# Kernel optimization log

Measured on AMD Instinct MI355X. Metric: run time of the kernel, lower is better.

The kernel has to match this reference:

```python
import jax, jax.numpy as jnp
import numpy as np

NUM_EMB = 8192
EMB_DIM = 32
LATENT = 1024
COMMIT = 0.25
CB_COST = 1.0


def _l2norm(x, eps=1e-12):
    # matches torch F.normalize: x / max(||x||, eps)
    n = jnp.sqrt(jnp.sum(x * x, axis=-1, keepdims=True))
    return x / jnp.maximum(n, eps)


def setup_inputs() -> dict:
    key = jax.random.key(0)
    k = jax.random.split(key, 6)
    B = 32768
    s_in = 1.0 / np.sqrt(LATENT)
    s_out = 1.0 / np.sqrt(EMB_DIM)
    return {
        "z_e": jax.random.normal(k[0], (B, LATENT), jnp.float32),
        "in_w": jax.random.uniform(k[1], (EMB_DIM, LATENT), jnp.float32, -s_in, s_in),
        "in_b": jax.random.uniform(k[2], (EMB_DIM,), jnp.float32, -s_in, s_in),
        "out_w": jax.random.uniform(k[3], (LATENT, EMB_DIM), jnp.float32, -s_out, s_out),
        "out_b": jax.random.uniform(k[4], (LATENT,), jnp.float32, -s_out, s_out),
        "codebook": jax.random.normal(k[5], (NUM_EMB, EMB_DIM), jnp.float32),
    }


def reference(z_e, in_w, in_b, out_w, out_b, codebook):
    # in_proj: [B, LATENT] -> [B, EMB_DIM]
    ze = z_e @ in_w.T + in_b
    zn = _l2norm(ze)                      # [B, E]
    wn = _l2norm(codebook)                # [Z, E]
    # squared euclidean distance between normalized vectors
    dist = (jnp.sum(zn * zn, axis=1, keepdims=True)
            - 2.0 * (zn @ wn.T)
            + jnp.sum(wn * wn, axis=1))   # [B, Z]
    idx = jnp.argmin(dist, axis=1)        # [B]
    z_q = codebook[idx]                   # [B, E] (unnormalized codebook lookup)
    enc_loss = jnp.mean((ze - jax.lax.stop_gradient(z_q)) ** 2)
    cb_loss = jnp.mean((z_q - jax.lax.stop_gradient(ze)) ** 2)
    loss = CB_COST * cb_loss + COMMIT * enc_loss
    # straight-through estimator
    z_st = ze + jax.lax.stop_gradient(z_q - ze)
    out = z_st @ out_w.T + out_b          # [B, LATENT]
    return out, loss, enc_loss, cb_loss, idx, ze
```

## Files before the change

kernel.cpp:

```cpp
#include <hip/hip_runtime.h>
#include <hip/hip_bf16.h>

#define B_SZ    32768
#define LAT     1024
#define EMB     32
#define ZCB     8192
#define NSPL    8
#define RESC_CAP 32768
#define EPS_MARGIN 2e-4f

#define OFF_LOSS  ((size_t)B_SZ * LAT)
#define OFF_ENC   (OFF_LOSS + 1)
#define OFF_CB    (OFF_LOSS + 2)
#define OFF_IDX   (OFF_LOSS + 3)
#define OFF_ZE    (OFF_IDX + B_SZ)

#define WS_PZE    0
#define WS_PB1    0
#define WS_PB2    262144
#define WS_PL15   524288
#define WS_CAND   1048576
#define WS_OTH    1081344
#define WS_ZEA    2097152
#define WS_ZNPK   3145728
#define WS_WPK    4194304
#define WS_IDXT   4456448
#define WS_CNT    4489216
#define WS_LIST   4489217
#define WS_LPART  4521985

typedef float  f32x4  __attribute__((ext_vector_type(4)));
typedef short  short8 __attribute__((ext_vector_type(8)));

__device__ __forceinline__ unsigned short f2bf(float x) {
    unsigned u = __float_as_uint(x);
    u += 0x7FFF + ((u >> 16) & 1);
    return (unsigned short)(u >> 16);
}
__device__ __forceinline__ float bf2f(unsigned short h) {
    return __uint_as_float(((unsigned)h) << 16);
}

__global__ __launch_bounds__(256) void knorm(const float* __restrict__ cb,
                                             short* __restrict__ wpk) {
    int e = threadIdx.x;
    int r = threadIdx.y;
    int row = blockIdx.x * 8 + r;
    float v = cb[row * EMB + e];
    float s = v * v;
    #pragma unroll
    for (int m = 16; m >= 1; m >>= 1) s += __shfl_xor(s, m, 64);
    float n = fmaxf(sqrtf(s), 1e-12f);
    float w = v / n;
    unsigned short h = f2bf(w);
    unsigned short l = f2bf(w - bf2f(h));
    wpk[row * 64 + e]      = (short)h;
    wpk[row * 64 + 32 + e] = (short)l;
}

#define KZB 64
#define KZS 68
__global__ __launch_bounds__(256) void kze2(const float* __restrict__ z_e,
                                            const float* __restrict__ in_w,
                                            float* __restrict__ pze) {
    __shared__ float zs[128 * KZS];
    __shared__ float wt[KZB * 32];
    int tid = threadIdx.x;
    size_t row0 = (size_t)blockIdx.x * 128;
    int ks = blockIdx.y;
    int rs = tid >> 2;
    int eg = tid & 3;
    int E  = eg * 8;

    float acc[2][8];
    #pragma unroll
    for (int i = 0; i < 2; ++i)
        #pragma unroll
        for (int j = 0; j < 8; ++j) acc[i][j] = 0.f;

    for (int c = 0; c < 512 / KZB; ++c) {
        int kb = ks * 512 + c * KZB;
        __syncthreads();
        #pragma unroll
        for (int i = 0; i < 8; ++i) {
            int t = tid + i * 256;
            int r = t >> 4, c4 = t & 15;
            float4 v = *(const float4*)(z_e + (row0 + r) * LAT + kb + c4 * 4);
            *(float4*)&zs[r * KZS + c4 * 4] = v;
        }
        #pragma unroll
        for (int i = 0; i < 2; ++i) {
            int t = tid + i * 256;
            int e = t >> 4, k4 = t & 15;
            float4 v = *(const float4*)(in_w + (size_t)e * LAT + kb + k4 * 4);
            float vv[4] = {v.x, v.y, v.z, v.w};
            #pragma unroll
            for (int j = 0; j < 4; ++j) {
                int k = k4 * 4 + j;
                wt[k * 32 + (e ^ ((k & 7) << 2))] = vv[j];
            }
        }
        __syncthreads();
        #pragma unroll 4
        for (int kq = 0; kq < KZB / 4; ++kq) {
            int k0 = kq * 4;
            float4 za = *(const float4*)&zs[rs * KZS + k0];
            float4 zb = *(const float4*)&zs[(rs + 64) * KZS + k0];
            float zav[4] = {za.x, za.y, za.z, za.w};
            float zbv[4] = {zb.x, zb.y, zb.z, zb.w};
            #pragma unroll
            for (int i = 0; i < 4; ++i) {
                int k = k0 + i;
                int sw = (k & 7) << 2;
                float4 w0 = *(const float4*)&wt[k * 32 + (E ^ sw)];
                float4 w1 = *(const float4*)&wt[k * 32 + ((E + 4) ^ sw)];
                float wa[8] = {w0.x, w0.y, w0.z, w0.w, w1.x, w1.y, w1.z, w1.w};
                #pragma unroll
                for (int j = 0; j < 8; ++j) {
                    acc[0][j] = fmaf(zav[i], wa[j], acc[0][j]);
                    acc[1][j] = fmaf(zbv[i], wa[j], acc[1][j]);
                }
            }
        }
    }
    size_t rb = ((size_t)ks * B_SZ + row0);
    float* p0 = pze + (rb + rs) * EMB + E;
    float* p1 = pze + (rb + rs + 64) * EMB + E;
    *(float4*)p0       = make_float4(acc[0][0], acc[0][1], acc[0][2], acc[0][3]);
    *(float4*)(p0 + 4) = make_float4(acc[0][4], acc[0][5], acc[0][6], acc[0][7]);
    *(float4*)p1       = make_float4(acc[1][0], acc[1][1], acc[1][2], acc[1][3]);
    *(float4*)(p1 + 4) = make_float4(acc[1][4], acc[1][5], acc[1][6], acc[1][7]);
}

__global__ __launch_bounds__(256) void kprep(const float* __restrict__ pze,
                                             const float* __restrict__ in_b,
                                             float* __restrict__ ze_out,
                                             float* __restrict__ ze_a,
                                             short* __restrict__ znpk) {
    int tid = threadIdx.x;
    size_t row = (size_t)blockIdx.x * 64 + (tid >> 2);
    int eg = tid & 3;
    const float* p0 = pze + row * 32 + eg * 8;
    const float* p1 = p0 + (size_t)B_SZ * 32;
    float4 a0 = *(const float4*)p0, a1 = *(const float4*)(p0 + 4);
    float4 b0 = *(const float4*)p1, b1 = *(const float4*)(p1 + 4);
    float4 c0 = *(const float4*)(in_b + eg * 8), c1 = *(const float4*)(in_b + eg * 8 + 4);
    float v[8];
    v[0] = a0.x + b0.x + c0.x; v[1] = a0.y + b0.y + c0.y;
    v[2] = a0.z + b0.z + c0.z; v[3] = a0.w + b0.w + c0.w;
    v[4] = a1.x + b1.x + c1.x; v[5] = a1.y + b1.y + c1.y;
    v[6] = a1.z + b1.z + c1.z; v[7] = a1.w + b1.w + c1.w;
    float nn = 0.f;
    #pragma unroll
    for (int i = 0; i < 8; ++i) nn = fmaf(v[i], v[i], nn);
    nn += __shfl_xor(nn, 1, 64);
    nn += __shfl_xor(nn, 2, 64);
    float n = fmaxf(sqrtf(nn), 1e-12f);

    *(float4*)(ze_a + row * 32 + eg * 8)     = make_float4(v[0], v[1], v[2], v[3]);
    *(float4*)(ze_a + row * 32 + eg * 8 + 4) = make_float4(v[4], v[5], v[6], v[7]);
    #pragma unroll
    for (int i = 0; i < 8; ++i) ze_out[row * 32 + eg * 8 + i] = v[i];

    short8 hv, lv;
    #pragma unroll
    for (int i = 0; i < 8; ++i) {
        float x = v[i] / n;
        unsigned short h = f2bf(x);
        unsigned short l = f2bf(x - bf2f(h));
        hv[i] = (short)h; lv[i] = (short)l;
    }
    *(short8*)(znpk + row * 64 + eg * 8)      = hv;
    *(short8*)(znpk + row * 64 + 32 + eg * 8) = lv;
}

__global__ __launch_bounds__(256) void kdistM(const short* __restrict__ znpk,
                                              const short* __restrict__ wpk,
                                              float* __restrict__ pb1,
                                              float* __restrict__ pb2,
                                              int*   __restrict__ pl15) {
    int tid = threadIdx.x;
    int wave = tid >> 6, l = tid & 63;
    int l15 = l & 15, g = l >> 4;
    size_t rowbase = (size_t)blockIdx.x * 256 + wave * 64;
    int s = blockIdx.y;

    short8 zh[4], zl[4];
    #pragma unroll
    for (int rt = 0; rt < 4; ++rt) {
        const short8* p = (const short8*)(znpk + (rowbase + rt * 16 + l15) * 64 + g * 8);
        zh[rt] = p[0];
        zl[rt] = p[4];
    }
    f32x4 zero4 = {0.f, 0.f, 0.f, 0.f};
    float bb1[16];
    #pragma unroll
    for (int i = 0; i < 16; ++i) bb1[i] = -1e30f;

    const short* wbase = wpk + ((size_t)s * 1024 + l15) * 64 + g * 8;
    for (int t = 0; t < 64; ++t) {
        const short8* wp = (const short8*)(wbase + (size_t)t * 1024);
        short8 bh = wp[0];
        short8 bl = wp[4];
        #pragma unroll
        for (int rt = 0; rt < 4; ++rt) {
            f32x4 acc = __builtin_amdgcn_mfma_f32_16x16x32_bf16(zh[rt], bh, zero4, 0, 0, 0);
            acc = __builtin_amdgcn_mfma_f32_16x16x32_bf16(zl[rt], bh, acc, 0, 0, 0);
            acc = __builtin_amdgcn_mfma_f32_16x16x32_bf16(zh[rt], bl, acc, 0, 0, 0);
            #pragma unroll
            for (int r = 0; r < 4; ++r) {
                int slot = rt * 4 + r;
                bb1[slot] = fmaxf(bb1[slot], acc[r]);
            }
        }
    }
    #pragma unroll
    for (int slot = 0; slot < 16; ++slot) {
        float B1 = bb1[slot], B2 = -1e30f;
        int ID = l15;
        #pragma unroll
        for (int m = 1; m <= 8; m <<= 1) {
            float ob1 = __shfl_xor(B1, m, 64);
            float ob2 = __shfl_xor(B2, m, 64);
            int   oid = __shfl_xor(ID, m, 64);
            float mn = fminf(B1, ob1);
            B2 = fmaxf(fmaxf(B2, ob2), mn);
            bool take = (ob1 > B1) || (ob1 == B1 && oid < ID);
            B1 = take ? ob1 : B1;
            ID = take ? oid : ID;
        }
        if (l15 == 0) {
            size_t row = rowbase + (size_t)(slot >> 2) * 16 + g * 4 + (slot & 3);
            pb1[(size_t)s * B_SZ + row] = B1;
            pb2[(size_t)s * B_SZ + row] = B2;
            pl15[(size_t)s * B_SZ + row] = ID;
        }
    }
}

__global__ __launch_bounds__(256) void kmergeArg(const float* __restrict__ pb1,
                                                 const float* __restrict__ pb2,
                                                 const int* __restrict__ pl15,
                                                 int* __restrict__ cand,
                                                 float* __restrict__ oth) {
    int row = blockIdx.x * 256 + threadIdx.x;
    float best1 = pb1[row], best2 = pb2[row];
    int c = pl15[row], wsn = 0;
    #pragma unroll
    for (int s = 1; s < NSPL; ++s) {
        float b  = pb1[(size_t)s * B_SZ + row];
        float sb = pb2[(size_t)s * B_SZ + row];
        int   li = pl15[(size_t)s * B_SZ + row];
        float mn = fminf(best1, b);
        best2 = fmaxf(fmaxf(best2, sb), mn);
        if (b > best1) { best1 = b; c = li; wsn = s; }
    }
    cand[row] = wsn * 16 + c;
    oth[row] = best2;
}

__global__ __launch_bounds__(256) void krecover(const float* __restrict__ ze_a,
                                                const float* __restrict__ cb,
                                                const int* __restrict__ cand,
                                                const float* __restrict__ oth,
                                                int* __restrict__ idxt,
                                                int* __restrict__ cnt,
                                                int* __restrict__ list) {
    int tid = threadIdx.x;
    int l = tid & 63;
    int gl = l & 7;
    int gj = l >> 3;
    int row = (blockIdx.x * 256 + tid) >> 6;
    int c = cand[row];
    int s = c >> 4, lc = c & 15;
    float4 z = *(const float4*)(ze_a + (size_t)row * 32 + gl * 4);
    float zz = fmaf(z.x, z.x, fmaf(z.y, z.y, fmaf(z.z, z.z, z.w * z.w)));
    zz += __shfl_xor(zz, 1, 64);
    zz += __shfl_xor(zz, 2, 64);
    zz += __shfl_xor(zz, 4, 64);
    float zinv = 1.f / fmaxf(sqrtf(zz), 1e-12f);
    z.x *= zinv; z.y *= zinv; z.z *= zinv; z.w *= zinv;

    float best = -1e30f; int bi = 0;
    #pragma unroll
    for (int b = 0; b < 8; ++b) {
        int t = b * 8 + gj;
        int j = s * 1024 + t * 16 + lc;
        float4 w = *(const float4*)(cb + (size_t)j * 32 + gl * 4);
        float w2 = fmaf(w.x, w.x, fmaf(w.y, w.y, fmaf(w.z, w.z, w.w * w.w)));
        float dt = fmaf(z.x, w.x, fmaf(z.y, w.y, fmaf(z.z, w.z, z.w * w.w)));
        w2 += __shfl_xor(w2, 1, 64); dt += __shfl_xor(dt, 1, 64);
        w2 += __shfl_xor(w2, 2, 64); dt += __shfl_xor(dt, 2, 64);
        w2 += __shfl_xor(w2, 4, 64); dt += __shfl_xor(dt, 4, 64);
        float inv = 1.f / fmaxf(sqrtf(w2), 1e-12f);
        float m = dt * inv - 0.5f * (w2 * inv * inv);
        if (m > best || (m == best && j < bi)) { best = m; bi = j; }
    }
    #pragma unroll
    for (int mk = 8; mk <= 32; mk <<= 1) {
        float ob = __shfl_xor(best, mk, 64);
        int   oi = __shfl_xor(bi, mk, 64);
        bool take = (ob > best) || (ob == best && oi < bi);
        best = take ? ob : best;
        bi   = take ? oi : bi;
    }
    if (l == 0) {
        idxt[row] = bi;
        if (best - (oth[row] - 0.5f) < EPS_MARGIN) {
            int p = atomicAdd(cnt, 1);
            if (p < RESC_CAP) list[p] = row;
        }
    }
}

__global__ __launch_bounds__(256) void krescore(const float* __restrict__ ze_a,
                                                const float* __restrict__ cb,
                                                int* __restrict__ idxt,
                                                const int* __restrict__ cnt,
                                                const int* __restrict__ list) {
    __shared__ float bvs[4];
    __shared__ int   bis[4];
    int tid = threadIdx.x;
    int wave = tid >> 6, l = tid & 63;
    int gl = l & 7;
    int gj = l >> 3;
    int n = *cnt; if (n > RESC_CAP) n = RESC_CAP;
    for (int ii = blockIdx.x; ii < n; ii += gridDim.x) {
        int row = list[ii];
        float4 z = *(const float4*)(ze_a + (size_t)row * 32 + gl * 4);
        float zz = fmaf(z.x, z.x, fmaf(z.y, z.y, fmaf(z.z, z.z, z.w * z.w)));
        zz += __shfl_xor(zz, 1, 64);
        zz += __shfl_xor(zz, 2, 64);
        zz += __shfl_xor(zz, 4, 64);
        float zinv = 1.f / fmaxf(sqrtf(zz), 1e-12f);
        z.x *= zinv; z.y *= zinv; z.z *= zinv; z.w *= zinv;

        float best = -1e30f; int bi = 0;
        int jbase = wave * 2048 + gj;
        for (int b = 0; b < 32; ++b) {
            float w2v[8], dtv[8];
            #pragma unroll
            for (int cc = 0; cc < 8; ++cc) {
                int j = jbase + (b * 8 + cc) * 8;
                float4 w = *(const float4*)(cb + (size_t)j * 32 + gl * 4);
                w2v[cc] = fmaf(w.x, w.x, fmaf(w.y, w.y, fmaf(w.z, w.z, w.w * w.w)));
                dtv[cc] = fmaf(z.x, w.x, fmaf(z.y, w.y, fmaf(z.z, w.z, z.w * w.w)));
            }
            #pragma unroll
            for (int cc = 0; cc < 8; ++cc) {
                w2v[cc] += __shfl_xor(w2v[cc], 1, 64);
                dtv[cc] += __shfl_xor(dtv[cc], 1, 64);
            }
            #pragma unroll
            for (int cc = 0; cc < 8; ++cc) {
                w2v[cc] += __shfl_xor(w2v[cc], 2, 64);
                dtv[cc] += __shfl_xor(dtv[cc], 2, 64);
            }
            #pragma unroll
            for (int cc = 0; cc < 8; ++cc) {
                w2v[cc] += __shfl_xor(w2v[cc], 4, 64);
                dtv[cc] += __shfl_xor(dtv[cc], 4, 64);
            }
            #pragma unroll
            for (int cc = 0; cc < 8; ++cc) {
                int j = jbase + (b * 8 + cc) * 8;
                float inv = 1.f / fmaxf(sqrtf(w2v[cc]), 1e-12f);
                float m = dtv[cc] * inv - 0.5f * (w2v[cc] * inv * inv);
                if (m > best || (m == best && j < bi)) { best = m; bi = j; }
            }
        }
        #pragma unroll
        for (int mk = 8; mk <= 32; mk <<= 1) {
            float ob = __shfl_xor(best, mk, 64);
            int   oi = __shfl_xor(bi, mk, 64);
            bool take = (ob > best) || (ob == best && oi < bi);
            best = take ? ob : best;
            bi   = take ? oi : bi;
        }
        if (l == 0) { bvs[wave] = best; bis[wave] = bi; }
        __syncthreads();
        if (tid == 0) {
            float B = bvs[0]; int I = bis[0];
            #pragma unroll
            for (int w2i = 1; w2i < 4; ++w2i) {
                float ob = bvs[w2i]; int oi = bis[w2i];
                if (ob > B || (ob == B && oi < I)) { B = ob; I = oi; }
            }
            idxt[row] = I;
        }
        __syncthreads();
    }
}

__global__ __launch_bounds__(256) void kfinal(const int* __restrict__ idxt,
                                              const float* __restrict__ ze,
                                              const float* __restrict__ cb,
                                              float* __restrict__ out_idx,
                                              float* __restrict__ lpart) {
    int tid = threadIdx.x;
    int row = blockIdx.x * 256 + tid;
    int bidx = idxt[row];
    out_idx[row] = (float)bidx;

    const float4* zq4 = (const float4*)(cb + (size_t)bidx * EMB);
    const float4* ze4 = (const float4*)(ze + (size_t)row * EMB);
    float sq = 0.f;
    #pragma unroll
    for (int i = 0; i < 8; ++i) {
        float4 q = zq4[i], z = ze4[i];
        float dx = z.x - q.x, dy = z.y - q.y, dz = z.z - q.z, dw = z.w - q.w;
        sq += (dx * dx + dy * dy) + (dz * dz + dw * dw);
    }
    #pragma unroll
    for (int m = 1; m <= 32; m <<= 1) sq += __shfl_xor(sq, m, 64);
    __shared__ float red[4];
    if ((tid & 63) == 0) red[tid >> 6] = sq;
    __syncthreads();
    if (tid == 0) lpart[blockIdx.x] = (red[0] + red[1]) + (red[2] + red[3]);
}

__global__ void kloss(const float* __restrict__ lpart, float* __restrict__ dout) {
    float v = lpart[threadIdx.x];
    #pragma unroll
    for (int m = 1; m <= 32; m <<= 1) v += __shfl_xor(v, m, 64);
    __shared__ float tmp[2];
    if ((threadIdx.x & 63) == 0) tmp[threadIdx.x >> 6] = v;
    __syncthreads();
    if (threadIdx.x == 0) {
        float enc = (tmp[0] + tmp[1]) / (float)(B_SZ * EMB);
        dout[OFF_LOSS] = 1.0f * enc + 0.25f * enc;
        dout[OFF_ENC]  = enc;
        dout[OFF_CB]   = enc;
    }
}

__global__ __launch_bounds__(256) void kout(const float* __restrict__ ze_a,
                                            const int* __restrict__ idxt,
                                            const float* __restrict__ cb,
                                            const float* __restrict__ out_w,
                                            const float* __restrict__ out_b,
                                            float* __restrict__ out) {
    __shared__ float zsh[128 * EMB];
    __shared__ int ish[128];
    int tid = threadIdx.x;
    int col = blockIdx.x * 512 + tid * 2;
    size_t row0 = (size_t)blockIdx.y * 128;
    if (tid < 128) ish[tid] = idxt[row0 + tid];
    __syncthreads();
    #pragma unroll
    for (int i = 0; i < 4; ++i) {
        int flat = i * 256 + tid;
        int r = flat >> 3, q = flat & 7;
        float4 zv = *(const float4*)(ze_a + (row0 + r) * EMB + q * 4);
        float4 qv = *(const float4*)(cb + (size_t)ish[r] * EMB + q * 4);
        float4 o;
        o.x = zv.x + (qv.x - zv.x); o.y = zv.y + (qv.y - zv.y);
        o.z = zv.z + (qv.z - zv.z); o.w = zv.w + (qv.w - zv.w);
        *(float4*)&zsh[r * EMB + q * 4] = o;
    }
    float wa[32], wb[32];
    {
        const float4* wa4 = (const float4*)(out_w + (size_t)col * EMB);
        const float4* wb4 = (const float4*)(out_w + (size_t)(col + 1) * EMB);
        #pragma unroll
        for (int i = 0; i < 8; ++i) {
            float4 a = wa4[i]; wa[4*i]=a.x; wa[4*i+1]=a.y; wa[4*i+2]=a.z; wa[4*i+3]=a.w;
            float4 b = wb4[i]; wb[4*i]=b.x; wb[4*i+1]=b.y; wb[4*i+2]=b.z; wb[4*i+3]=b.w;
        }
    }
    float b0 = out_b[col], b1 = out_b[col + 1];
    __syncthreads();
    for (int rr = 0; rr < 128; ++rr) {
        const float4* zr4 = (const float4*)(zsh + rr * EMB);
        float a0 = b0, a1 = b1;
        #pragma unroll
        for (int q = 0; q < 8; ++q) {
            float4 z = zr4[q];
            a0 = fmaf(z.x, wa[4*q],   a0); a1 = fmaf(z.x, wb[4*q],   a1);
            a0 = fmaf(z.y, wa[4*q+1], a0); a1 = fmaf(z.y, wb[4*q+1], a1);
            a0 = fmaf(z.z, wa[4*q+2], a0); a1 = fmaf(z.z, wb[4*q+2], a1);
            a0 = fmaf(z.w, wa[4*q+3], a0); a1 = fmaf(z.w, wb[4*q+3], a1);
        }
        float2 o; o.x = a0; o.y = a1;
        *(float2*)(out + (row0 + rr) * LAT + col) = o;
    }
}

extern "C" void kernel_launch(void* const* d_in, const int* in_sizes, int n_in,
                              void* d_out, int out_size, void* d_ws, size_t ws_size,
                              hipStream_t stream) {
    const float* z_e   = (const float*)d_in[0];
    const float* in_w  = (const float*)d_in[1];
    const float* in_b  = (const float*)d_in[2];
    const float* out_w = (const float*)d_in[3];
    const float* out_b = (const float*)d_in[4];
    const float* cb    = (const float*)d_in[5];

    float* out = (float*)d_out;
    float* ws  = (float*)d_ws;
    float* pze   = ws + WS_PZE;
    float* pb1   = ws + WS_PB1;
    float* pb2   = ws + WS_PB2;
    int*   pl15  = (int*)(ws + WS_PL15);
    int*   cand  = (int*)(ws + WS_CAND);
    float* oth   = ws + WS_OTH;
    float* ze_a  = ws + WS_ZEA;
    short* znpk  = (short*)(ws + WS_ZNPK);
    short* wpk   = (short*)(ws + WS_WPK);
    int*   idxt  = (int*)(ws + WS_IDXT);
    int*   cnt   = (int*)(ws + WS_CNT);
    int*   list  = (int*)(ws + WS_LIST);
    float* lpart = ws + WS_LPART;

    hipMemsetAsync((void*)cnt, 0, sizeof(int), stream);
    knorm    <<<dim3(ZCB / 8), dim3(32, 8), 0, stream>>>(cb, wpk);
    kze2     <<<dim3(B_SZ / 128, 2), 256, 0, stream>>>(z_e, in_w, pze);
    kprep    <<<dim3(B_SZ / 64), 256, 0, stream>>>(pze, in_b, out + OFF_ZE, ze_a, znpk);
    kdistM   <<<dim3(B_SZ / 256, NSPL), 256, 0, stream>>>(znpk, wpk, pb1, pb2, pl15);
    kmergeArg<<<dim3(B_SZ / 256), 256, 0, stream>>>(pb1, pb2, pl15, cand, oth);
    krecover <<<dim3(B_SZ / 4), 256, 0, stream>>>(ze_a, cb, cand, oth, idxt, cnt, list);
    krescore <<<dim3(512), 256, 0, stream>>>(ze_a, cb, idxt, cnt, list);
    kfinal   <<<dim3(B_SZ / 256), 256, 0, stream>>>(idxt, ze_a, cb, out + OFF_IDX, lpart);
    kloss    <<<1, 128, 0, stream>>>(lpart, out);
    kout     <<<dim3(2, B_SZ / 128), 256, 0, stream>>>(ze_a, idxt, cb, out_w, out_b, out);
}
```

Baseline: 271.6 us.

## Prefetch codebook tiles in distance loop, shrink projection tiles, fold counter reset

After: 274.3 us. No clear change (+1.0%).

```diff
diff --git a/kernel.cpp b/kernel.cpp
--- a/kernel.cpp
+++ b/kernel.cpp
@@ -6,6 +6,7 @@
 #define EMB     32
 #define ZCB     8192
 #define NSPL    8
+#define CPS     (ZCB / NSPL)
 #define RESC_CAP 32768
 #define EPS_MARGIN 2e-4f
 
@@ -19,8 +20,8 @@
 #define WS_PB1    0
 #define WS_PB2    262144
 #define WS_PL15   524288
-#define WS_CAND   1048576
-#define WS_OTH    1081344
+#define WS_CAND   786432
+#define WS_OTH    819200
 #define WS_ZEA    2097152
 #define WS_ZNPK   3145728
 #define WS_WPK    4194304
@@ -63,26 +64,24 @@
 __global__ __launch_bounds__(256) void kze2(const float* __restrict__ z_e,
                                             const float* __restrict__ in_w,
                                             float* __restrict__ pze) {
-    __shared__ float zs[128 * KZS];
+    __shared__ float zs[64 * KZS];
     __shared__ float wt[KZB * 32];
     int tid = threadIdx.x;
-    size_t row0 = (size_t)blockIdx.x * 128;
+    size_t row0 = (size_t)blockIdx.x * 64;
     int ks = blockIdx.y;
     int rs = tid >> 2;
     int eg = tid & 3;
     int E  = eg * 8;
 
-    float acc[2][8];
-    #pragma unroll
-    for (int i = 0; i < 2; ++i)
-        #pragma unroll
-        for (int j = 0; j < 8; ++j) acc[i][j] = 0.f;
+    float acc[8];
+    #pragma unroll
+    for (int j = 0; j < 8; ++j) acc[j] = 0.f;
 
     for (int c = 0; c < 512 / KZB; ++c) {
         int kb = ks * 512 + c * KZB;
         __syncthreads();
         #pragma unroll
-        for (int i = 0; i < 8; ++i) {
+        for (int i = 0; i < 4; ++i) {
             int t = tid + i * 256;
             int r = t >> 4, c4 = t & 15;
             float4 v = *(const float4*)(z_e + (row0 + r) * LAT + kb + c4 * 4);
@@ -105,9 +104,7 @@
         for (int kq = 0; kq < KZB / 4; ++kq) {
             int k0 = kq * 4;
             float4 za = *(const float4*)&zs[rs * KZS + k0];
-            float4 zb = *(const float4*)&zs[(rs + 64) * KZS + k0];
             float zav[4] = {za.x, za.y, za.z, za.w};
-            float zbv[4] = {zb.x, zb.y, zb.z, zb.w};
             #pragma unroll
             for (int i = 0; i < 4; ++i) {
                 int k = k0 + i;
@@ -116,20 +113,15 @@
                 float4 w1 = *(const float4*)&wt[k * 32 + ((E + 4) ^ sw)];
                 float wa[8] = {w0.x, w0.y, w0.z, w0.w, w1.x, w1.y, w1.z, w1.w};
                 #pragma unroll
-                for (int j = 0; j < 8; ++j) {
-                    acc[0][j] = fmaf(zav[i], wa[j], acc[0][j]);
-                    acc[1][j] = fmaf(zbv[i], wa[j], acc[1][j]);
-                }
-            }
-        }
-    }
-    size_t rb = ((size_t)ks * B_SZ + row0);
+                for (int j = 0; j < 8; ++j)
+                    acc[j] = fmaf(zav[i], wa[j], acc[j]);
+            }
+        }
+    }
+    size_t rb = (size_t)ks * B_SZ + row0;
     float* p0 = pze + (rb + rs) * EMB + E;
-    float* p1 = pze + (rb + rs + 64) * EMB + E;
-    *(float4*)p0       = make_float4(acc[0][0], acc[0][1], acc[0][2], acc[0][3]);
-    *(float4*)(p0 + 4) = make_float4(acc[0][4], acc[0][5], acc[0][6], acc[0][7]);
-    *(float4*)p1       = make_float4(acc[1][0], acc[1][1], acc[1][2], acc[1][3]);
-    *(float4*)(p1 + 4) = make_float4(acc[1][4], acc[1][5], acc[1][6], acc[1][7]);
+    *(float4*)p0       = make_float4(acc[0], acc[1], acc[2], acc[3]);
+    *(float4*)(p0 + 4) = make_float4(acc[4], acc[5], acc[6], acc[7]);
 }
 
 __global__ __launch_bounds__(256) void kprep(const float* __restrict__ pze,
@@ -197,22 +189,29 @@
     #pragma unroll
     for (int i = 0; i < 16; ++i) bb1[i] = -1e30f;
 
-    const short* wbase = wpk + ((size_t)s * 1024 + l15) * 64 + g * 8;
-    for (int t = 0; t < 64; ++t) {
-        const short8* wp = (const short8*)(wbase + (size_t)t * 1024);
-        short8 bh = wp[0];
-        short8 bl = wp[4];
+    const short* wbase = wpk + ((size_t)s * CPS + l15) * 64 + g * 8;
+    const short8* wp0 = (const short8*)wbase;
+    short8 bh = wp0[0];
+    short8 bl = wp0[4];
+    for (int t = 0; t < CPS / 16; ++t) {
+        short8 nbh = bh, nbl = bl;
+        if (t + 1 < CPS / 16) {
+            const short8* wn = (const short8*)(wbase + (size_t)(t + 1) * 1024);
+            nbh = wn[0];
+            nbl = wn[4];
+        }
         #pragma unroll
         for (int rt = 0; rt < 4; ++rt) {
-            f32x4 acc = __builtin_amdgcn_mfma_f32_16x16x32_bf16(zh[rt], bh, zero4, 0, 0, 0);
-            acc = __builtin_amdgcn_mfma_f32_16x16x32_bf16(zl[rt], bh, acc, 0, 0, 0);
-            acc = __builtin_amdgcn_mfma_f32_16x16x32_bf16(zh[rt], bl, acc, 0, 0, 0);
+            f32x4 c1 = __builtin_amdgcn_mfma_f32_16x16x32_bf16(zh[rt], bh, zero4, 0, 0, 0);
+            f32x4 c2 = __builtin_amdgcn_mfma_f32_16x16x32_bf16(zh[rt], bl, zero4, 0, 0, 0);
+            c2 = __builtin_amdgcn_mfma_f32_16x16x32_bf16(zl[rt], bh, c2, 0, 0, 0);
             #pragma unroll
             for (int r = 0; r < 4; ++r) {
                 int slot = rt * 4 + r;
-                bb1[slot] = fmaxf(bb1[slot], acc[r]);
-            }
-        }
+                bb1[slot] = fmaxf(bb1[slot], c1[r] + c2[r]);
+            }
+        }
+        bh = nbh; bl = nbl;
     }
     #pragma unroll
     for (int slot = 0; slot < 16; ++slot) {
@@ -242,7 +241,9 @@
                                                  const float* __restrict__ pb2,
                                                  const int* __restrict__ pl15,
                                                  int* __restrict__ cand,
-                                                 float* __restrict__ oth) {
+                                                 float* __restrict__ oth,
+                                                 int* __restrict__ cnt) {
+    if (blockIdx.x == 0 && threadIdx.x == 0) *cnt = 0;
     int row = blockIdx.x * 256 + threadIdx.x;
     float best1 = pb1[row], best2 = pb2[row];
     int c = pl15[row], wsn = 0;
@@ -283,9 +284,9 @@
 
     float best = -1e30f; int bi = 0;
     #pragma unroll
-    for (int b = 0; b < 8; ++b) {
+    for (int b = 0; b < CPS / 16 / 8; ++b) {
         int t = b * 8 + gj;
-        int j = s * 1024 + t * 16 + lc;
+        int j = s * CPS + t * 16 + lc;
         float4 w = *(const float4*)(cb + (size_t)j * 32 + gl * 4);
         float w2 = fmaf(w.x, w.x, fmaf(w.y, w.y, fmaf(w.z, w.z, w.w * w.w)));
         float dt = fmaf(z.x, w.x, fmaf(z.y, w.y, fmaf(z.z, w.z, z.w * w.w)));
@@ -512,12 +513,11 @@
     int*   list  = (int*)(ws + WS_LIST);
     float* lpart = ws + WS_LPART;
 
-    hipMemsetAsync((void*)cnt, 0, sizeof(int), stream);
     knorm    <<<dim3(ZCB / 8), dim3(32, 8), 0, stream>>>(cb, wpk);
-    kze2     <<<dim3(B_SZ / 128, 2), 256, 0, stream>>>(z_e, in_w, pze);
+    kze2     <<<dim3(B_SZ / 64, 2), 256, 0, stream>>>(z_e, in_w, pze);
     kprep    <<<dim3(B_SZ / 64), 256, 0, stream>>>(pze, in_b, out + OFF_ZE, ze_a, znpk);
     kdistM   <<<dim3(B_SZ / 256, NSPL), 256, 0, stream>>>(znpk, wpk, pb1, pb2, pl15);
-    kmergeArg<<<dim3(B_SZ / 256), 256, 0, stream>>>(pb1, pb2, pl15, cand, oth);
+    kmergeArg<<<dim3(B_SZ / 256), 256, 0, stream>>>(pb1, pb2, pl15, cand, oth, cnt);
     krecover <<<dim3(B_SZ / 4), 256, 0, stream>>>(ze_a, cb, cand, oth, idxt, cnt, list);
     krescore <<<dim3(512), 256, 0, stream>>>(ze_a, cb, idxt, cnt, list);
     kfinal   <<<dim3(B_SZ / 256), 256, 0, stream>>>(idxt, ze_a, cb, out + OFF_IDX, lpart);
```
